# Performance work log

Measured on AMD Instinct MI355X. Metric: run time of the kernel, lower is better.

## Reference

```python
import jax, jax.numpy as jnp
import numpy as np

EPS = 1e-7
B, F, C, H, W, D = 2, 2, 64, 32, 104, 96


def _pix_homog(h, w):
    ys, xs = jnp.meshgrid(jnp.arange(h, dtype=jnp.float32),
                          jnp.arange(w, dtype=jnp.float32), indexing='ij')
    return jnp.stack([xs.ravel(), ys.ravel(), jnp.ones(h * w, jnp.float32)], 0)  # [3, H*W]


def setup_inputs() -> dict:
    key = jax.random.key(0)
    k1, k2 = jax.random.split(key)
    current_feats = jax.random.normal(k1, (B, C, H, W), jnp.float32)
    lookup_feats = jax.random.normal(k2, (B, F, C, H, W), jnp.float32)

    rng = np.random.RandomState(0)
    # intrinsics at matching (feature) resolution, monodepth2-style
    Km = np.eye(4, dtype=np.float32)
    Km[0, 0] = 0.58 * W
    Km[1, 1] = 1.92 * H
    Km[0, 2] = 0.5 * W
    Km[1, 2] = 0.5 * H
    K = np.tile(Km[None], (B, 1, 1))
    invK = np.linalg.inv(K).astype(np.float32)

    # near-identity relative poses (small rotation perturbation + small translation)
    poses = np.tile(np.eye(4, dtype=np.float32)[None, None], (B, F, 1, 1))
    poses[:, :, :3, :3] += 0.02 * rng.randn(B, F, 3, 3).astype(np.float32)
    poses[:, :, :3, 3] = 0.1 * rng.randn(B, F, 3).astype(np.float32)

    depth_bins = jnp.linspace(0.1, 20.0, D, dtype=jnp.float32)
    return {
        'current_feats': current_feats,
        'lookup_feats': lookup_feats,
        'poses': jnp.asarray(poses),
        'K': jnp.asarray(K),
        'invK': jnp.asarray(invK),
        'depth_bins': depth_bins,
    }


def _grid_sample_zeros(lfT, gx, gy, h, w):
    """Bilinear grid_sample, align_corners=True, padding_mode='zeros'.
    lfT: [B,F,H,W,C]; gx,gy: [B,F,D,H,W] in pixel coords. -> [B,F,D,H,W,C]"""
    x0 = jnp.floor(gx)
    y0 = jnp.floor(gy)
    x0i = x0.astype(jnp.int32)
    y0i = y0.astype(jnp.int32)
    wx1 = gx - x0
    wy1 = gy - y0
    wx0 = 1.0 - wx1
    wy0 = 1.0 - wy1
    bb = jnp.arange(lfT.shape[0])[:, None, None, None, None]
    ff = jnp.arange(lfT.shape[1])[None, :, None, None, None]

    def corner(yi, xi, wgt):
        m = ((xi >= 0) & (xi < w) & (yi >= 0) & (yi < h)).astype(lfT.dtype)
        xc = jnp.clip(xi, 0, w - 1)
        yc = jnp.clip(yi, 0, h - 1)
        v = lfT[bb, ff, yc, xc]                      # [B,F,D,H,W,C]
        return v * (m * wgt)[..., None]

    return (corner(y0i, x0i, wy0 * wx0) + corner(y0i, x0i + 1, wy0 * wx1)
            + corner(y0i + 1, x0i, wy1 * wx0) + corner(y0i + 1, x0i + 1, wy1 * wx1))


def reference(current_feats, lookup_feats, poses, K, invK, depth_bins):
    b, c, h, w = current_feats.shape
    f = lookup_feats.shape[1]
    d = depth_bins.shape[0]

    # Backproject: world points for each hypothesised depth plane
    pix = _pix_homog(h, w)                                   # [3, HW]
    cam = jnp.einsum('bij,jn->bin', invK[:, :3, :3], pix)    # [B,3,HW]
    pts = depth_bins[None, :, None, None] * cam[:, None]     # [B,D,3,HW]
    world = jnp.concatenate([pts, jnp.ones((b, d, 1, h * w), pts.dtype)], 2)  # [B,D,4,HW]

    # Project into each lookup frame
    P = jnp.einsum('bij,bfjk->bfik', K, poses)[:, :, :3, :]  # [B,F,3,4]
    cpts = jnp.einsum('bfij,bdjn->bfdin', P, world)          # [B,F,D,3,HW]
    xy = cpts[:, :, :, :2] / (cpts[:, :, :, 2:3] + EPS)      # pixel coords [B,F,D,2,HW]
    xy = xy.reshape(b, f, d, 2, h, w)
    gx, gy = xy[:, :, :, 0], xy[:, :, :, 1]                  # [B,F,D,H,W]

    # edge mask (detach in original -> stop_gradient)
    sx, sy = jax.lax.stop_gradient(gx), jax.lax.stop_gradient(gy)
    edge = ((sx >= 2.0) & (sx <= w - 2) & (sy >= 2.0) & (sy <= h - 2)).astype(jnp.float32)
    interior = jnp.zeros((h, w), jnp.float32).at[2:-2, 2:-2].set(1.0)
    edge_mask = edge * interior                               # [B,F,D,H,W]

    # warp lookup features and L1-diff against current features
    lfT = lookup_feats.transpose(0, 1, 3, 4, 2)               # [B,F,H,W,C]
    warped = _grid_sample_zeros(lfT, gx, gy, h, w)            # [B,F,D,H,W,C]
    cur = current_feats.transpose(0, 2, 3, 1)                 # [B,H,W,C]
    diffs = jnp.abs(warped - cur[:, None, None]).mean(-1) * edge_mask  # [B,F,D,H,W]

    # skip lookup frames whose pose is all-zero
    valid = (poses.sum((-2, -1)) != 0).astype(jnp.float32)    # [B,F]
    diffs = diffs * valid[:, :, None, None, None]

    cost = diffs.sum(1)                                        # [B,D,H,W]
    counts = (diffs > 0).astype(jnp.float32).sum(1)
    cost = cost / (counts + EPS)

    # set missing values to per-pixel max over depth bins
    missing = (cost == 0.0)
    cmax = cost.max(1, keepdims=True)
    cost = jnp.where(missing, cmax, cost)
    return cost
```

## Files before the change

### kernel.cpp

```cpp
#include <hip/hip_runtime.h>
#include <math.h>

constexpr int B_ = 2, F_ = 2, C_ = 64, H_ = 32, W_ = 104, D_ = 96;
constexpr int HW_ = H_ * W_;
#define EPSF 1e-7f

constexpr size_t LFT_ELEMS  = (size_t)B_ * F_ * HW_ * C_;
constexpr size_t CURT_OFF_F = LFT_ELEMS / 2;

constexpr int NT_BLKS = (HW_ / 32) * (C_ / 32) * (B_ * F_ + B_);
constexpr int PXB   = 4;
constexpr int XT_   = W_ / PXB;
constexpr int DPAD  = D_ + 1;
constexpr int DPADI = D_ + 4;

template<int CTRL>
__device__ __forceinline__ float dpp_add(float x) {
    int y = __builtin_amdgcn_update_dpp(0, __float_as_int(x), CTRL, 0xf, 0xf, true);
    return x + __int_as_float(y);
}
__device__ __forceinline__ float group16_sum(float s) {
    s = dpp_add<0xB1>(s);
    s = dpp_add<0x4E>(s);
    s = dpp_add<0x141>(s);
    s = dpp_add<0x140>(s);
    return s;
}

__device__ __forceinline__ ushort f2bf(float f) {
    unsigned u = __float_as_uint(f);
    u += 0x7FFFu + ((u >> 16) & 1u);
    return (ushort)(u >> 16);
}
__device__ __forceinline__ float4 bf4(uint2 q) {
    return make_float4(__uint_as_float(q.x << 16),
                       __uint_as_float(q.x & 0xffff0000u),
                       __uint_as_float(q.y << 16),
                       __uint_as_float(q.y & 0xffff0000u));
}

__global__ __launch_bounds__(256) void prep_kernel(
        const float* __restrict__ cur, const float* __restrict__ lf,
        float* __restrict__ ws) {
    __shared__ float tile[32][33];
    int bid = blockIdx.x;
    int slice = bid / 208;
    int rem   = bid % 208;
    int nb = rem % 104, cb = rem / 104;
    const float* inS = (slice < B_ * F_)
        ? lf  + (size_t)slice * C_ * HW_
        : cur + (size_t)(slice - B_ * F_) * C_ * HW_;
    int t = threadIdx.x;
    int tx = t & 31, ty = t >> 5;
    int n0 = nb * 32, c0 = cb * 32;
    #pragma unroll
    for (int k = 0; k < 32; k += 8)
        tile[ty + k][tx] = inS[(size_t)(c0 + ty + k) * HW_ + n0 + tx];
    __syncthreads();
    if (slice < B_ * F_) {
        ushort* outS = (ushort*)ws + (size_t)slice * HW_ * C_;
        #pragma unroll
        for (int k = 0; k < 32; k += 8)
            outS[(size_t)(n0 + ty + k) * C_ + c0 + tx] = f2bf(tile[tx][ty + k]);
    } else {
        float* outS = ws + CURT_OFF_F + (size_t)(slice - B_ * F_) * HW_ * C_;
        #pragma unroll
        for (int k = 0; k < 32; k += 8)
            outS[(size_t)(n0 + ty + k) * C_ + c0 + tx] = tile[tx][ty + k];
    }
}

__global__ __launch_bounds__(256, 6) void mega_kernel(
        const float* __restrict__ poses, const float* __restrict__ K,
        const float* __restrict__ invK, const float* __restrict__ depth_bins,
        const float* __restrict__ ws, float* __restrict__ out) {
    int t   = threadIdx.x;
    int bid = blockIdx.x;
    int xt  = bid % XT_;  int r = bid / XT_;
    int y   = r % H_;
    int b   = r / H_;

    if (y < 2 || y >= H_ - 2) {
        for (int k = t; k < PXB * D_; k += 256) {
            int d = k >> 2, px = k & 3;
            out[((size_t)(b * D_ + d) * H_ + y) * W_ + xt * PXB + px] = 0.0f;
        }
        return;
    }

    __shared__ alignas(16) int offsL[F_][PXB][DPADI];
    __shared__ float4 wtsL [F_][PXB][DPAD];
    __shared__ float  costb[PXB][DPAD];
    __shared__ float  pmax[32][PXB];
    __shared__ float  cmaxb[PXB];

    {
        int pxA = t & 3;
        int xA  = xt * PXB + pxA;
        const float* iK = invK + (size_t)b * 16;
        float xf = (float)xA, yf = (float)y;
        float cam0 = __fmul_rn(iK[0], xf); cam0 = __fmaf_rn(iK[1], yf, cam0); cam0 = __fmaf_rn(iK[2],  1.0f, cam0);
        float cam1 = __fmul_rn(iK[4], xf); cam1 = __fmaf_rn(iK[5], yf, cam1); cam1 = __fmaf_rn(iK[6],  1.0f, cam1);
        float cam2 = __fmul_rn(iK[8], xf); cam2 = __fmaf_rn(iK[9], yf, cam2); cam2 = __fmaf_rn(iK[10], 1.0f, cam2);
        bool interior = (xA >= 2) && (xA <= W_ - 3);

        #pragma unroll
        for (int f = 0; f < F_; ++f) {
            const float* Kb   = K + (size_t)b * 16;
            const float* pose = poses + (size_t)(b * F_ + f) * 16;
            float P[12];
            #pragma unroll
            for (int i = 0; i < 3; ++i) {
                #pragma unroll
                for (int k = 0; k < 4; ++k) {
                    float acc = __fmul_rn(Kb[i*4+0], pose[0*4+k]);
                    acc = __fmaf_rn(Kb[i*4+1], pose[1*4+k], acc);
                    acc = __fmaf_rn(Kb[i*4+2], pose[2*4+k], acc);
                    acc = __fmaf_rn(Kb[i*4+3], pose[3*4+k], acc);
                    P[i*4+k] = acc;
                }
            }
            float vs = 0.f;
            #pragma unroll
            for (int j = 0; j < 16; ++j) vs += pose[j];
            bool valid = (vs != 0.f);

            #pragma unroll
            for (int k = 0; k < 2; ++k) {
                int idx = t + 256 * k;
                if (idx < PXB * D_) {
                    int dd = idx >> 2;
                    float depth = depth_bins[dd];
                    float p0 = __fmul_rn(depth, cam0);
                    float p1 = __fmul_rn(depth, cam1);
                    float p2 = __fmul_rn(depth, cam2);
                    float c0 = __fmul_rn(P[0], p0); c0 = __fmaf_rn(P[1], p1, c0); c0 = __fmaf_rn(P[2],  p2, c0); c0 = __fmaf_rn(P[3],  1.0f, c0);
                    float c1 = __fmul_rn(P[4], p0); c1 = __fmaf_rn(P[5], p1, c1); c1 = __fmaf_rn(P[6],  p2, c1); c1 = __fmaf_rn(P[7],  1.0f, c1);
                    float c2 = __fmul_rn(P[8], p0); c2 = __fmaf_rn(P[9], p1, c2); c2 = __fmaf_rn(P[10], p2, c2); c2 = __fmaf_rn(P[11], 1.0f, c2);
                    float denom = __fadd_rn(c2, EPSF);
                    float gx = c0 / denom;
                    float gy = c1 / denom;
                    bool m = valid && interior && (gx >= 2.0f) && (gx <= (float)(W_ - 2))
                                               && (gy >= 2.0f) && (gy <= (float)(H_ - 2));
                    if (m) {
                        float x0f = floorf(gx), y0f = floorf(gy);
                        int   x0  = (int)x0f,   y0  = (int)y0f;
                        float wx1 = gx - x0f, wy1 = gy - y0f;
                        float wx0 = 1.f - wx1, wy0 = 1.f - wy1;
                        wtsL[f][pxA][dd] = make_float4(wy0 * wx0, wy0 * wx1,
                                                       wy1 * wx0, wy1 * wx1);
                        offsL[f][pxA][dd] = (y0 * W_ + x0) * C_;
                    } else {
                        offsL[f][pxA][dd] = -1;
                        wtsL[f][pxA][dd] = make_float4(0.f, 0.f, 0.f, 0.f);
                    }
                }
            }
        }
    }
    __syncthreads();

    {
        int lane = t & 15, px = (t >> 4) & 3, half = t >> 6;
        int x = xt * PXB + px;
        const float4 cv = *(const float4*)(ws + CURT_OFF_F
                            + ((size_t)((b * H_ + y) * W_ + x)) * C_ + lane * 4);
        const ushort* lfbase = (const ushort*)ws;
        const ushort* lf0a = lfbase + (size_t)(b * F_ + 0) * HW_ * C_ + lane * 4;
        const ushort* lf0b = lf0a + W_ * C_;
        const ushort* lf1a = lfbase + (size_t)(b * F_ + 1) * HW_ * C_ + lane * 4;
        const ushort* lf1b = lf1a + W_ * C_;

        float4 cc0[4], cc1[4];
        int oprev0 = -1, oprev1 = -1;
        #pragma unroll
        for (int k = 0; k < 4; ++k)
            cc0[k] = cc1[k] = make_float4(0.f, 0.f, 0.f, 0.f);

        int dbeg = half * (D_ / 4);
        for (int ki4 = 0; ki4 < D_ / 16; ++ki4) {
            int dc4 = dbeg + ki4 * 4;
            int4 oq0 = *(const int4*)&offsL[0][px][dc4];
            int4 oq1 = *(const int4*)&offsL[1][px][dc4];
            int oa0[4] = {oq0.x, oq0.y, oq0.z, oq0.w};
            int oa1[4] = {oq1.x, oq1.y, oq1.z, oq1.w};

            #pragma unroll
            for (int j = 0; j < 4; ++j) {
                int dc = dc4 + j;
                int    oc0 = oa0[j],          oc1 = oa1[j];
                float4 wc0 = wtsL[0][px][dc], wc1 = wtsL[1][px][dc];

                float costsum = 0.f, counts = 0.f;
                {
                    bool m = (oc0 >= 0);
                    if (m && oc0 != oprev0) {
                        uint2 q0 = *(const uint2*)(lf0a + oc0);
                        uint2 q1 = *(const uint2*)(lf0a + oc0 + C_);
                        uint2 q2 = *(const uint2*)(lf0b + oc0);
                        uint2 q3 = *(const uint2*)(lf0b + oc0 + C_);
                        cc0[0] = bf4(q0); cc0[1] = bf4(q1); cc0[2] = bf4(q2); cc0[3] = bf4(q3);
                        oprev0 = oc0;
                    }
                    float a0 = __fmaf_rn(cc0[0].x, wc0.x, __fmaf_rn(cc0[1].x, wc0.y, __fmaf_rn(cc0[2].x, wc0.z, __fmaf_rn(cc0[3].x, wc0.w, -cv.x))));
                    float a1 = __fmaf_rn(cc0[0].y, wc0.x, __fmaf_rn(cc0[1].y, wc0.y, __fmaf_rn(cc0[2].y, wc0.z, __fmaf_rn(cc0[3].y, wc0.w, -cv.y))));
                    float a2 = __fmaf_rn(cc0[0].z, wc0.x, __fmaf_rn(cc0[1].z, wc0.y, __fmaf_rn(cc0[2].z, wc0.z, __fmaf_rn(cc0[3].z, wc0.w, -cv.z))));
                    float a3 = __fmaf_rn(cc0[0].w, wc0.x, __fmaf_rn(cc0[1].w, wc0.y, __fmaf_rn(cc0[2].w, wc0.z, __fmaf_rn(cc0[3].w, wc0.w, -cv.w))));
                    float s = (fabsf(a0) + fabsf(a1)) + (fabsf(a2) + fabsf(a3));
                    s = group16_sum(s);
                    float diff = __fmul_rn(s, 1.0f / 64.0f) * (m ? 1.0f : 0.0f);
                    costsum += diff;
                    counts  += (diff > 0.f) ? 1.0f : 0.0f;
                }
                {
                    bool m = (oc1 >= 0);
                    if (m && oc1 != oprev1) {
                        uint2 q0 = *(const uint2*)(lf1a + oc1);
                        uint2 q1 = *(const uint2*)(lf1a + oc1 + C_);
                        uint2 q2 = *(const uint2*)(lf1b + oc1);
                        uint2 q3 = *(const uint2*)(lf1b + oc1 + C_);
                        cc1[0] = bf4(q0); cc1[1] = bf4(q1); cc1[2] = bf4(q2); cc1[3] = bf4(q3);
                        oprev1 = oc1;
                    }
                    float a0 = __fmaf_rn(cc1[0].x, wc1.x, __fmaf_rn(cc1[1].x, wc1.y, __fmaf_rn(cc1[2].x, wc1.z, __fmaf_rn(cc1[3].x, wc1.w, -cv.x))));
                    float a1 = __fmaf_rn(cc1[0].y, wc1.x, __fmaf_rn(cc1[1].y, wc1.y, __fmaf_rn(cc1[2].y, wc1.z, __fmaf_rn(cc1[3].y, wc1.w, -cv.y))));
                    float a2 = __fmaf_rn(cc1[0].z, wc1.x, __fmaf_rn(cc1[1].z, wc1.y, __fmaf_rn(cc1[2].z, wc1.z, __fmaf_rn(cc1[3].z, wc1.w, -cv.z))));
                    float a3 = __fmaf_rn(cc1[0].w, wc1.x, __fmaf_rn(cc1[1].w, wc1.y, __fmaf_rn(cc1[2].w, wc1.z, __fmaf_rn(cc1[3].w, wc1.w, -cv.w))));
                    float s = (fabsf(a0) + fabsf(a1)) + (fabsf(a2) + fabsf(a3));
                    s = group16_sum(s);
                    float diff = __fmul_rn(s, 1.0f / 64.0f) * (m ? 1.0f : 0.0f);
                    costsum += diff;
                    counts  += (diff > 0.f) ? 1.0f : 0.0f;
                }
                float cost = costsum * __builtin_amdgcn_rcpf(__fadd_rn(counts, EPSF));
                if (lane == 0) costb[px][dc] = cost;
            }
        }
    }
    __syncthreads();

    {
        int j = t >> 2, px = t & 3;
        float v[3];
        if (t < 128) {
            float pm = 0.f;
            #pragma unroll
            for (int k = 0; k < 3; ++k) {
                v[k] = costb[px][j + 32 * k];
                pm = fmaxf(pm, v[k]);
            }
            pmax[j][px] = pm;
        }
        __syncthreads();
        if (t < PXB) {
            float cm = 0.f;
            #pragma unroll
            for (int jj = 0; jj < 32; ++jj) cm = fmaxf(cm, pmax[jj][t]);
            cmaxb[t] = cm;
        }
        __syncthreads();
        if (t < 128) {
            float cm = cmaxb[px];
            int x = xt * PXB + px;
            #pragma unroll
            for (int k = 0; k < 3; ++k) {
                int d = j + 32 * k;
                out[((size_t)(b * D_ + d) * H_ + y) * W_ + x] = (v[k] == 0.0f) ? cm : v[k];
            }
        }
    }
}

extern "C" void kernel_launch(void* const* d_in, const int* in_sizes, int n_in,
                              void* d_out, int out_size, void* d_ws, size_t ws_size,
                              hipStream_t stream) {
    const float* cur        = (const float*)d_in[0];
    const float* lf         = (const float*)d_in[1];
    const float* poses      = (const float*)d_in[2];
    const float* K          = (const float*)d_in[3];
    const float* invK       = (const float*)d_in[4];
    const float* depth_bins = (const float*)d_in[5];
    float* out = (float*)d_out;
    float* ws  = (float*)d_ws;

    prep_kernel<<<NT_BLKS, 256, 0, stream>>>(cur, lf, ws);
    mega_kernel<<<B_ * H_ * XT_, 256, 0, stream>>>(poses, K, invK, depth_bins, ws, out);
}
```

Baseline: 103.2 us.

## Split depth range across two blocks and move max-fill into a fixup kernel

Each mega_kernel block now handles half of the depth bins for its 4-pixel tile, which doubles the grid size and raises the occupancy hint. Because the per-pixel max over depth now spans two blocks, the shared-memory reduction is removed: costs are written straight to global memory, and a new fixup_kernel rereads all depth bins per pixel to fill zero entries with the max. This trades more parallelism and smaller LDS use for an extra kernel launch and an extra read/write pass over the output. Per-pixel projection setup (pose/K products) is also duplicated across the two blocks.

```diff
diff --git a/kernel.cpp b/kernel.cpp
--- a/kernel.cpp
+++ b/kernel.cpp
@@ -11,8 +11,9 @@
 constexpr int NT_BLKS = (HW_ / 32) * (C_ / 32) * (B_ * F_ + B_);
 constexpr int PXB   = 4;
 constexpr int XT_   = W_ / PXB;
-constexpr int DPAD  = D_ + 1;
-constexpr int DPADI = D_ + 4;
+constexpr int DL_   = 48;
+constexpr int DPAD  = DL_ + 1;
+constexpr int DPADI = DL_ + 4;
 
 template<int CTRL>
 __device__ __forceinline__ float dpp_add(float x) {
@@ -70,19 +71,21 @@
     }
 }
 
-__global__ __launch_bounds__(256, 6) void mega_kernel(
+__global__ __launch_bounds__(256, 8) void mega_kernel(
         const float* __restrict__ poses, const float* __restrict__ K,
         const float* __restrict__ invK, const float* __restrict__ depth_bins,
         const float* __restrict__ ws, float* __restrict__ out) {
     int t   = threadIdx.x;
     int bid = blockIdx.x;
     int xt  = bid % XT_;  int r = bid / XT_;
+    int dhalf = r & 1;    r >>= 1;
     int y   = r % H_;
     int b   = r / H_;
+    int d0g = dhalf * DL_;
 
     if (y < 2 || y >= H_ - 2) {
-        for (int k = t; k < PXB * D_; k += 256) {
-            int d = k >> 2, px = k & 3;
+        for (int k = t; k < PXB * DL_; k += 256) {
+            int d = d0g + (k >> 2), px = k & 3;
             out[((size_t)(b * D_ + d) * H_ + y) * W_ + xt * PXB + px] = 0.0f;
         }
         return;
@@ -90,9 +93,6 @@
 
     __shared__ alignas(16) int offsL[F_][PXB][DPADI];
     __shared__ float4 wtsL [F_][PXB][DPAD];
-    __shared__ float  costb[PXB][DPAD];
-    __shared__ float  pmax[32][PXB];
-    __shared__ float  cmaxb[PXB];
 
     {
         int pxA = t & 3;
@@ -125,35 +125,31 @@
             for (int j = 0; j < 16; ++j) vs += pose[j];
             bool valid = (vs != 0.f);
 
-            #pragma unroll
-            for (int k = 0; k < 2; ++k) {
-                int idx = t + 256 * k;
-                if (idx < PXB * D_) {
-                    int dd = idx >> 2;
-                    float depth = depth_bins[dd];
-                    float p0 = __fmul_rn(depth, cam0);
-                    float p1 = __fmul_rn(depth, cam1);
-                    float p2 = __fmul_rn(depth, cam2);
-                    float c0 = __fmul_rn(P[0], p0); c0 = __fmaf_rn(P[1], p1, c0); c0 = __fmaf_rn(P[2],  p2, c0); c0 = __fmaf_rn(P[3],  1.0f, c0);
-                    float c1 = __fmul_rn(P[4], p0); c1 = __fmaf_rn(P[5], p1, c1); c1 = __fmaf_rn(P[6],  p2, c1); c1 = __fmaf_rn(P[7],  1.0f, c1);
-                    float c2 = __fmul_rn(P[8], p0); c2 = __fmaf_rn(P[9], p1, c2); c2 = __fmaf_rn(P[10], p2, c2); c2 = __fmaf_rn(P[11], 1.0f, c2);
-                    float denom = __fadd_rn(c2, EPSF);
-                    float gx = c0 / denom;
-                    float gy = c1 / denom;
-                    bool m = valid && interior && (gx >= 2.0f) && (gx <= (float)(W_ - 2))
-                                               && (gy >= 2.0f) && (gy <= (float)(H_ - 2));
-                    if (m) {
-                        float x0f = floorf(gx), y0f = floorf(gy);
-                        int   x0  = (int)x0f,   y0  = (int)y0f;
-                        float wx1 = gx - x0f, wy1 = gy - y0f;
-                        float wx0 = 1.f - wx1, wy0 = 1.f - wy1;
-                        wtsL[f][pxA][dd] = make_float4(wy0 * wx0, wy0 * wx1,
-                                                       wy1 * wx0, wy1 * wx1);
-                        offsL[f][pxA][dd] = (y0 * W_ + x0) * C_;
-                    } else {
-                        offsL[f][pxA][dd] = -1;
-                        wtsL[f][pxA][dd] = make_float4(0.f, 0.f, 0.f, 0.f);
-                    }
+            if (t < PXB * DL_) {
+                int dd = t >> 2;
+                float depth = depth_bins[d0g + dd];
+                float p0 = __fmul_rn(depth, cam0);
+                float p1 = __fmul_rn(depth, cam1);
+                float p2 = __fmul_rn(depth, cam2);
+                float c0 = __fmul_rn(P[0], p0); c0 = __fmaf_rn(P[1], p1, c0); c0 = __fmaf_rn(P[2],  p2, c0); c0 = __fmaf_rn(P[3],  1.0f, c0);
+                float c1 = __fmul_rn(P[4], p0); c1 = __fmaf_rn(P[5], p1, c1); c1 = __fmaf_rn(P[6],  p2, c1); c1 = __fmaf_rn(P[7],  1.0f, c1);
+                float c2 = __fmul_rn(P[8], p0); c2 = __fmaf_rn(P[9], p1, c2); c2 = __fmaf_rn(P[10], p2, c2); c2 = __fmaf_rn(P[11], 1.0f, c2);
+                float denom = __fadd_rn(c2, EPSF);
+                float gx = c0 / denom;
+                float gy = c1 / denom;
+                bool m = valid && interior && (gx >= 2.0f) && (gx <= (float)(W_ - 2))
+                                           && (gy >= 2.0f) && (gy <= (float)(H_ - 2));
+                if (m) {
+                    float x0f = floorf(gx), y0f = floorf(gy);
+                    int   x0  = (int)x0f,   y0  = (int)y0f;
+                    float wx1 = gx - x0f, wy1 = gy - y0f;
+                    float wx0 = 1.f - wx1, wy0 = 1.f - wy1;
+                    wtsL[f][pxA][dd] = make_float4(wy0 * wx0, wy0 * wx1,
+                                                   wy1 * wx0, wy1 * wx1);
+                    offsL[f][pxA][dd] = (y0 * W_ + x0) * C_;
+                } else {
+                    offsL[f][pxA][dd] = -1;
+                    wtsL[f][pxA][dd] = make_float4(0.f, 0.f, 0.f, 0.f);
                 }
             }
         }
@@ -161,7 +157,7 @@
     __syncthreads();
 
     {
-        int lane = t & 15, px = (t >> 4) & 3, half = t >> 6;
+        int lane = t & 15, px = (t >> 4) & 3, quarter = t >> 6;
         int x = xt * PXB + px;
         const float4 cv = *(const float4*)(ws + CURT_OFF_F
                             + ((size_t)((b * H_ + y) * W_ + x)) * C_ + lane * 4);
@@ -177,8 +173,9 @@
         for (int k = 0; k < 4; ++k)
             cc0[k] = cc1[k] = make_float4(0.f, 0.f, 0.f, 0.f);
 
-        int dbeg = half * (D_ / 4);
-        for (int ki4 = 0; ki4 < D_ / 16; ++ki4) {
+        size_t outbase = ((size_t)(b * D_ + d0g) * H_ + y) * W_ + x;
+        int dbeg = quarter * (DL_ / 4);
+        for (int ki4 = 0; ki4 < DL_ / 16; ++ki4) {
             int dc4 = dbeg + ki4 * 4;
             int4 oq0 = *(const int4*)&offsL[0][px][dc4];
             int4 oq1 = *(const int4*)&offsL[1][px][dc4];
@@ -195,11 +192,10 @@
                 {
                     bool m = (oc0 >= 0);
                     if (m && oc0 != oprev0) {
-                        uint2 q0 = *(const uint2*)(lf0a + oc0);
-                        uint2 q1 = *(const uint2*)(lf0a + oc0 + C_);
-                        uint2 q2 = *(const uint2*)(lf0b + oc0);
-                        uint2 q3 = *(const uint2*)(lf0b + oc0 + C_);
-                        cc0[0] = bf4(q0); cc0[1] = bf4(q1); cc0[2] = bf4(q2); cc0[3] = bf4(q3);
+                        cc0[0] = bf4(*(const uint2*)(lf0a + oc0));
+                        cc0[1] = bf4(*(const uint2*)(lf0a + oc0 + C_));
+                        cc0[2] = bf4(*(const uint2*)(lf0b + oc0));
+                        cc0[3] = bf4(*(const uint2*)(lf0b + oc0 + C_));
                         oprev0 = oc0;
                     }
                     float a0 = __fmaf_rn(cc0[0].x, wc0.x, __fmaf_rn(cc0[1].x, wc0.y, __fmaf_rn(cc0[2].x, wc0.z, __fmaf_rn(cc0[3].x, wc0.w, -cv.x))));
@@ -215,11 +211,10 @@
                 {
                     bool m = (oc1 >= 0);
                     if (m && oc1 != oprev1) {
-                        uint2 q0 = *(const uint2*)(lf1a + oc1);
-                        uint2 q1 = *(const uint2*)(lf1a + oc1 + C_);
-                        uint2 q2 = *(const uint2*)(lf1b + oc1);
-                        uint2 q3 = *(const uint2*)(lf1b + oc1 + C_);
-                        cc1[0] = bf4(q0); cc1[1] = bf4(q1); cc1[2] = bf4(q2); cc1[3] = bf4(q3);
+                        cc1[0] = bf4(*(const uint2*)(lf1a + oc1));
+                        cc1[1] = bf4(*(const uint2*)(lf1a + oc1 + C_));
+                        cc1[2] = bf4(*(const uint2*)(lf1b + oc1));
+                        cc1[3] = bf4(*(const uint2*)(lf1b + oc1 + C_));
                         oprev1 = oc1;
                     }
                     float a0 = __fmaf_rn(cc1[0].x, wc1.x, __fmaf_rn(cc1[1].x, wc1.y, __fmaf_rn(cc1[2].x, wc1.z, __fmaf_rn(cc1[3].x, wc1.w, -cv.x))));
@@ -233,41 +228,27 @@
                     counts  += (diff > 0.f) ? 1.0f : 0.0f;
                 }
                 float cost = costsum * __builtin_amdgcn_rcpf(__fadd_rn(counts, EPSF));
-                if (lane == 0) costb[px][dc] = cost;
+                if (lane == 0) out[outbase + (size_t)dc * HW_] = cost;
             }
         }
     }
-    __syncthreads();
-
-    {
-        int j = t >> 2, px = t & 3;
-        float v[3];
-        if (t < 128) {
-            float pm = 0.f;
-            #pragma unroll
-            for (int k = 0; k < 3; ++k) {
-                v[k] = costb[px][j + 32 * k];
-                pm = fmaxf(pm, v[k]);
-            }
-            pmax[j][px] = pm;
-        }
-        __syncthreads();
-        if (t < PXB) {
-            float cm = 0.f;
-            #pragma unroll
-            for (int jj = 0; jj < 32; ++jj) cm = fmaxf(cm, pmax[jj][t]);
-            cmaxb[t] = cm;
-        }
-        __syncthreads();
-        if (t < 128) {
-            float cm = cmaxb[px];
-            int x = xt * PXB + px;
-            #pragma unroll
-            for (int k = 0; k < 3; ++k) {
-                int d = j + 32 * k;
-                out[((size_t)(b * D_ + d) * H_ + y) * W_ + x] = (v[k] == 0.0f) ? cm : v[k];
-            }
-        }
+}
+
+__global__ __launch_bounds__(128) void fixup_kernel(float* __restrict__ out) {
+    int by = blockIdx.x;
+    int b = by / H_, y = by % H_;
+    int x = threadIdx.x;
+    if (x >= W_) return;
+    size_t base = ((size_t)(b * D_) * H_ + y) * W_ + x;
+    float cm = 0.f;
+    #pragma unroll 8
+    for (int d = 0; d < D_; ++d)
+        cm = fmaxf(cm, out[base + (size_t)d * HW_]);
+    #pragma unroll 8
+    for (int d = 0; d < D_; ++d) {
+        size_t idx = base + (size_t)d * HW_;
+        float v = out[idx];
+        if (v == 0.0f) out[idx] = cm;
     }
 }
 
@@ -284,5 +265,6 @@
     float* ws  = (float*)d_ws;
 
     prep_kernel<<<NT_BLKS, 256, 0, stream>>>(cur, lf, ws);
-    mega_kernel<<<B_ * H_ * XT_, 256, 0, stream>>>(poses, K, invK, depth_bins, ws, out);
-}
+    mega_kernel<<<B_ * H_ * 2 * XT_, 256, 0, stream>>>(poses, K, invK, depth_bins, ws, out);
+    fixup_kernel<<<B_ * H_, 128, 0, stream>>>(out);
+}
```

Result: slower. 132.9 us (+28.8%).
